# Kernel optimization log

Hardware: AMD Instinct MI355X
Metric: run time of the kernel (lower is better)

The kernel has to match this reference:

```python
import jax, jax.numpy as jnp
import numpy as np

B, N, C = 32, 2248, 1024
D = 128            # bottleneck (down_size)
P = 200            # num_prompt_tokens
SCALE = D ** (-0.5)


def setup_inputs() -> dict:
    key = jax.random.key(0)
    k = jax.random.split(key, 5)
    return {
        "x": jax.random.normal(k[0], (B, N, C), dtype=jnp.float32),
        "W_down": jax.random.normal(k[1], (C, D), dtype=jnp.float32) * (C ** -0.5),
        "b_down": jax.random.normal(k[2], (D,), dtype=jnp.float32) * 0.01,
        "W_up": jax.random.normal(k[3], (D, C), dtype=jnp.float32) * (D ** -0.5),
        "b_up": jax.random.normal(k[4], (C,), dtype=jnp.float32) * 0.01,
        "gate": jnp.ones((), dtype=jnp.float32),
    }


def reference(x, W_down, b_down, W_up, b_up, gate):
    # down-projection + exact GELU (torch nn.GELU default is erf-based)
    down = jax.nn.gelu(jnp.einsum('bnc,cd->bnd', x, W_down) + b_down,
                       approximate=False)                      # [B, N, D]
    prompt_down = down[:, :P, :]                               # [B, P, D]
    token_down = down[:, P:, :]                                # [B, N-P, D]
    # prompt-token cross attention
    attn = jax.nn.softmax(
        jnp.einsum('bpd,btd->bpt', prompt_down, token_down) * SCALE, axis=-1)
    prompt_out = jnp.einsum('bpt,btd->bpd', attn, token_down)  # [B, P, D]
    combined = jnp.concatenate([prompt_out, token_down], axis=1)  # [B, N, D]
    up = jnp.einsum('bnd,dc->bnc', combined, W_up) + b_up      # [B, N, C]
    return gate * up
```

## Files before the change

kernel.cpp:

```cpp
#include <hip/hip_runtime.h>
#include <hip/hip_bf16.h>
#include <math.h>

#define B_   32
#define N_   2248
#define C_   1024
#define D_   128
#define P_   200
#define T_   2048
#define M_   (B_ * N_)
#define SCALE_ 0.08838834764831845f

typedef __bf16 bf16;
typedef __bf16 bf16x8 __attribute__((ext_vector_type(8)));
typedef __bf16 bf16x4 __attribute__((ext_vector_type(4)));
typedef float  f32x4  __attribute__((ext_vector_type(4)));
typedef unsigned int u32x4 __attribute__((ext_vector_type(4)));

#define VT_COL(dd, t) ((((((t) >> 3) ^ (((dd) >> 3) & 7)) << 3)) | ((t) & 7))

__global__ void k_prep(const float* __restrict__ Wd, const float* __restrict__ Wu,
                       bf16* __restrict__ WtD, bf16* __restrict__ WtU) {
    int i = blockIdx.x * 256 + threadIdx.x;
    if (i >= 131072) return;
    int d = i >> 10, k = i & 1023;
    WtD[i] = (bf16)Wd[k * 128 + d];
    int c = i >> 7, e = i & 127;
    WtU[i] = (bf16)Wu[e * 1024 + c];
}

__launch_bounds__(256, 3)
__global__ void k_down(const float* __restrict__ x, const bf16* __restrict__ WtD,
                       const float* __restrict__ bd, bf16* __restrict__ down) {
    __shared__ bf16 As[128][72];
    const int tid = threadIdx.x;
    const int lane = tid & 63, wid = tid >> 6;
    const int wm = wid >> 1, wn = wid & 1;
    const int li = lane & 15, lg = lane >> 4;
    const int m0 = blockIdx.x * 128;
    const bf16* Bp = WtD + (size_t)(wn * 64 + li) * C_ + lg * 8;

    f32x4 acc[4][4];
    const f32x4 zero = {0.f, 0.f, 0.f, 0.f};
#pragma unroll
    for (int i = 0; i < 4; i++)
#pragma unroll
        for (int j = 0; j < 4; j++) acc[i][j] = zero;

    for (int k0 = 0; k0 < C_; k0 += 64) {
        __syncthreads();
#pragma unroll
        for (int it = 0; it < 4; it++) {
            int ch = tid + it * 256;
            int r = ch >> 3, c8 = (ch & 7) * 8;
            const float* src = x + (size_t)(m0 + r) * C_ + k0 + c8;
            f32x4 v0 = *(const f32x4*)src;
            f32x4 v1 = *(const f32x4*)(src + 4);
            bf16x8 o;
            o[0] = (bf16)v0[0]; o[1] = (bf16)v0[1]; o[2] = (bf16)v0[2]; o[3] = (bf16)v0[3];
            o[4] = (bf16)v1[0]; o[5] = (bf16)v1[1]; o[6] = (bf16)v1[2]; o[7] = (bf16)v1[3];
            *(bf16x8*)&As[r][c8] = o;
        }
        __syncthreads();
#pragma unroll
        for (int kk = 0; kk < 2; kk++) {
            bf16x8 af[4], bf_[4];
#pragma unroll
            for (int f = 0; f < 4; f++)
                bf_[f] = *(const bf16x8*)(Bp + (size_t)(f * 16) * C_ + k0 + kk * 32);
#pragma unroll
            for (int f = 0; f < 4; f++)
                af[f] = *(const bf16x8*)&As[wm * 64 + f * 16 + li][kk * 32 + lg * 8];
#pragma unroll
            for (int fm = 0; fm < 4; fm++)
#pragma unroll
                for (int fn = 0; fn < 4; fn++)
                    acc[fm][fn] = __builtin_amdgcn_mfma_f32_16x16x32_bf16(
                        af[fm], bf_[fn], acc[fm][fn], 0, 0, 0);
        }
    }
#pragma unroll
    for (int fn = 0; fn < 4; fn++) {
        int col = wn * 64 + fn * 16 + li;
        float bias = bd[col];
#pragma unroll
        for (int fm = 0; fm < 4; fm++) {
            int rb = m0 + wm * 64 + fm * 16 + lg * 4;
#pragma unroll
            for (int r = 0; r < 4; r++) {
                float v = acc[fm][fn][r] + bias;
                float g = 0.5f * v * (1.0f + erff(v * 0.70710678118654752f));
                down[(size_t)(rb + r) * D_ + col] = (bf16)g;
            }
        }
    }
}

__launch_bounds__(256, 2)
__global__ void k_attn(const bf16* __restrict__ down, float* __restrict__ Opart,
                       float* __restrict__ Mpart, float* __restrict__ Lpart) {
    __shared__ bf16 Qs[64][136];
    __shared__ bf16 Ks[64][136];
    __shared__ bf16 Vt[128][72];
    __shared__ bf16 Ps[4][16][72];
    const int tid = threadIdx.x;
    const int lane = tid & 63, w = tid >> 6;
    const int li = lane & 15, lg = lane >> 4;
    const int b  = blockIdx.x >> 3;
    const int qt = (blockIdx.x >> 1) & 3;
    const int th = blockIdx.x & 1;
    const size_t base = (size_t)b * N_ * D_;
    const int tbase = P_ + th * 1024;

#pragma unroll
    for (int it = 0; it < 4; it++) {
        int ch = tid + it * 256;
        int r = ch >> 4, c8 = (ch & 15) * 8;
        *(u32x4*)&Qs[r][c8] = *(const u32x4*)(down + base + (size_t)(qt * 64 + r) * D_ + c8);
    }
    __syncthreads();
    bf16x8 qf[4];
#pragma unroll
    for (int kk = 0; kk < 4; kk++)
        qf[kk] = *(const bf16x8*)&Qs[w * 16 + li][kk * 32 + lg * 8];

    float m_run[4], l_run[4];
    f32x4 acc[8];
    const f32x4 zero = {0.f, 0.f, 0.f, 0.f};
#pragma unroll
    for (int r = 0; r < 4; r++) { m_run[r] = -3.0e38f; l_run[r] = 0.f; }
#pragma unroll
    for (int fn = 0; fn < 8; fn++) acc[fn] = zero;

    for (int tt = 0; tt < 16; tt++) {
        __syncthreads();
#pragma unroll
        for (int it = 0; it < 4; it++) {
            int ch = tid + it * 256;
            int r = ch >> 4, c8 = (ch & 15) * 8;
            u32x4 v = *(const u32x4*)(down + base + (size_t)(tbase + tt * 64 + r) * D_ + c8);
            *(u32x4*)&Ks[r][c8] = v;
            bf16 tmp[8];
            *(u32x4*)tmp = v;
#pragma unroll
            for (int j = 0; j < 8; j++) Vt[c8 + j][VT_COL(c8 + j, r)] = tmp[j];
        }
        __syncthreads();
        f32x4 s[4];
#pragma unroll
        for (int fn = 0; fn < 4; fn++) {
            s[fn] = zero;
#pragma unroll
            for (int kk = 0; kk < 4; kk++) {
                bf16x8 kf = *(const bf16x8*)&Ks[fn * 16 + li][kk * 32 + lg * 8];
                s[fn] = __builtin_amdgcn_mfma_f32_16x16x32_bf16(qf[kk], kf, s[fn], 0, 0, 0);
            }
            s[fn] *= SCALE_;
        }
#pragma unroll
        for (int r = 0; r < 4; r++) {
            float tmax = fmaxf(fmaxf(s[0][r], s[1][r]), fmaxf(s[2][r], s[3][r]));
#pragma unroll
            for (int off = 1; off < 16; off <<= 1)
                tmax = fmaxf(tmax, __shfl_xor(tmax, off, 64));
            float mnew = fmaxf(m_run[r], tmax);
            float corr = __expf(m_run[r] - mnew);
            m_run[r] = mnew;
            float psum = 0.f;
#pragma unroll
            for (int fn = 0; fn < 4; fn++) {
                float p = __expf(s[fn][r] - mnew);
                psum += p;
                Ps[w][lg * 4 + r][fn * 16 + li] = (bf16)p;
            }
#pragma unroll
            for (int off = 1; off < 16; off <<= 1)
                psum += __shfl_xor(psum, off, 64);
            l_run[r] = l_run[r] * corr + psum;
#pragma unroll
            for (int fn = 0; fn < 8; fn++) acc[fn][r] *= corr;
        }
#pragma unroll
        for (int kk = 0; kk < 2; kk++) {
            bf16x8 pf = *(const bf16x8*)&Ps[w][li][kk * 32 + lg * 8];
#pragma unroll
            for (int fn = 0; fn < 8; fn++) {
                int d = fn * 16 + li;
                bf16x8 vf = *(const bf16x8*)&Vt[d][VT_COL(d, kk * 32 + lg * 8)];
                acc[fn] = __builtin_amdgcn_mfma_f32_16x16x32_bf16(pf, vf, acc[fn], 0, 0, 0);
            }
        }
    }
#pragma unroll
    for (int r = 0; r < 4; r++) {
        int q = qt * 64 + w * 16 + lg * 4 + r;
        size_t ro = ((size_t)(b * 2 + th) * 256 + q) * 128;
#pragma unroll
        for (int fn = 0; fn < 8; fn++)
            Opart[ro + fn * 16 + li] = acc[fn][r];
        if (li == 0) {
            Mpart[(b * 2 + th) * 256 + q] = m_run[r];
            Lpart[(b * 2 + th) * 256 + q] = l_run[r];
        }
    }
}

__global__ void k_comb(const float* __restrict__ Opart, const float* __restrict__ Mpart,
                       const float* __restrict__ Lpart, bf16* __restrict__ pout) {
    int gid = blockIdx.x * 256 + threadIdx.x;
    if (gid >= (B_ * P_ * D_) / 4) return;
    int e = gid * 4;
    int row = e >> 7;
    int col = e & 127;
    int b = row / P_;
    int q = row - b * P_;
    int i1 = (b * 2 + 0) * 256 + q;
    int i2 = (b * 2 + 1) * 256 + q;
    float m1 = Mpart[i1], m2 = Mpart[i2];
    float l1 = Lpart[i1], l2 = Lpart[i2];
    float m = fmaxf(m1, m2);
    float a1 = __expf(m1 - m), a2 = __expf(m2 - m);
    float inv = 1.0f / (l1 * a1 + l2 * a2);
    f32x4 o1 = *(const f32x4*)&Opart[(size_t)i1 * 128 + col];
    f32x4 o2 = *(const f32x4*)&Opart[(size_t)i2 * 128 + col];
    bf16x4 o;
#pragma unroll
    for (int j = 0; j < 4; j++)
        o[j] = (bf16)((o1[j] * a1 + o2[j] * a2) * inv);
    *(bf16x4*)&pout[(size_t)row * 128 + col] = o;
}

__launch_bounds__(256, 3)
__global__ void k_up(const bf16* __restrict__ down, const bf16* __restrict__ pout,
                     const bf16* __restrict__ WtU, const float* __restrict__ bu,
                     const float* __restrict__ gate, float* __restrict__ out) {
    __shared__ bf16 As[128][136];
    const int tid = threadIdx.x;
    const int lane = tid & 63, wid = tid >> 6;
    const int wm = wid >> 1, wn = wid & 1;
    const int li = lane & 15, lg = lane >> 4;
    int bid = blockIdx.x;
    int wg = (bid & 7) * 562 + (bid >> 3);
    const int mt = wg >> 3, nt = wg & 7;
    const int m0 = mt * 128, n0 = nt * 128;
    const bf16* Bp = WtU + (size_t)(n0 + wn * 64 + li) * D_ + lg * 8;

#pragma unroll
    for (int it = 0; it < 8; it++) {
        int ch = tid + it * 256;
        int r = ch >> 4, c8 = (ch & 15) * 8;
        int m = m0 + r;
        int bb = m / N_;
        int n = m - bb * N_;
        const bf16* src = (n < P_) ? (pout + (size_t)(bb * P_ + n) * D_ + c8)
                                   : (down + (size_t)m * D_ + c8);
        *(u32x4*)&As[r][c8] = *(const u32x4*)src;
    }
    __syncthreads();

    f32x4 acc[4][4];
    const f32x4 zero = {0.f, 0.f, 0.f, 0.f};
#pragma unroll
    for (int i = 0; i < 4; i++)
#pragma unroll
        for (int j = 0; j < 4; j++) acc[i][j] = zero;

#pragma unroll
    for (int kk = 0; kk < 4; kk++) {
        bf16x8 af[4], bf_[4];
#pragma unroll
        for (int f = 0; f < 4; f++)
            bf_[f] = *(const bf16x8*)(Bp + (size_t)(f * 16) * D_ + kk * 32);
#pragma unroll
        for (int f = 0; f < 4; f++)
            af[f] = *(const bf16x8*)&As[wm * 64 + f * 16 + li][kk * 32 + lg * 8];
#pragma unroll
        for (int fm = 0; fm < 4; fm++)
#pragma unroll
            for (int fn = 0; fn < 4; fn++)
                acc[fm][fn] = __builtin_amdgcn_mfma_f32_16x16x32_bf16(
                    af[fm], bf_[fn], acc[fm][fn], 0, 0, 0);
    }

    float g = gate[0];
#pragma unroll
    for (int fn = 0; fn < 4; fn++) {
        int c = n0 + wn * 64 + fn * 16 + li;
        float bias = bu[c];
#pragma unroll
        for (int fm = 0; fm < 4; fm++) {
            int rb = m0 + wm * 64 + fm * 16 + lg * 4;
#pragma unroll
            for (int r = 0; r < 4; r++)
                out[(size_t)(rb + r) * C_ + c] = g * (acc[fm][fn][r] + bias);
        }
    }
}

extern "C" void kernel_launch(void* const* d_in, const int* in_sizes, int n_in,
                              void* d_out, int out_size, void* d_ws, size_t ws_size,
                              hipStream_t stream) {
    const float* x    = (const float*)d_in[0];
    const float* Wd   = (const float*)d_in[1];
    const float* bd   = (const float*)d_in[2];
    const float* Wu   = (const float*)d_in[3];
    const float* bu   = (const float*)d_in[4];
    const float* gate = (const float*)d_in[5];
    float* out = (float*)d_out;

    char* w = (char*)d_ws;
    bf16*  down  = (bf16*)w;
    bf16*  pout  = (bf16*)(w + 18415616);
    bf16*  WtD   = (bf16*)(w + 20054016);
    bf16*  WtU   = (bf16*)(w + 20316160);
    float* Opart = (float*)(w + 20578304);
    float* Mpart = (float*)(w + 28966912);
    float* Lpart = (float*)(w + 29032448);

    k_prep<<<512, 256, 0, stream>>>(Wd, Wu, WtD, WtU);
    k_down<<<M_ / 128, 256, 0, stream>>>(x, WtD, bd, down);
    k_attn<<<B_ * 8, 256, 0, stream>>>(down, Opart, Mpart, Lpart);
    k_comb<<<800, 256, 0, stream>>>(Opart, Mpart, Lpart, pout);
    k_up<<<(M_ / 128) * 8, 256, 0, stream>>>(down, pout, WtU, bu, gate, out);
}
```

Baseline: 267.4 us.

## Load GEMM operands directly from global and split attention keys four ways

The down and up projection kernels stop staging the A tile in shared memory. Each lane now loads its MFMA fragment straight from global memory (converting fp32 to bf16 in k_down), which removes the LDS writes and barriers. The risk is redundant global loads across the two column-warps and less coalesced access. The attention kernel splits the key range into four chunks instead of two and uses an XCD-aware block remap, doubling the grid to 512 blocks. The combine kernel merges four partials, and the workspace offsets grow to fit them.

```diff
diff --git a/kernel.cpp b/kernel.cpp
--- a/kernel.cpp
+++ b/kernel.cpp
@@ -32,13 +32,13 @@
 __launch_bounds__(256, 3)
 __global__ void k_down(const float* __restrict__ x, const bf16* __restrict__ WtD,
                        const float* __restrict__ bd, bf16* __restrict__ down) {
-    __shared__ bf16 As[128][72];
     const int tid = threadIdx.x;
     const int lane = tid & 63, wid = tid >> 6;
     const int wm = wid >> 1, wn = wid & 1;
     const int li = lane & 15, lg = lane >> 4;
     const int m0 = blockIdx.x * 128;
-    const bf16* Bp = WtD + (size_t)(wn * 64 + li) * C_ + lg * 8;
+    const float* Ap = x   + (size_t)(m0 + wm * 64 + li) * C_ + lg * 8;
+    const bf16*  Bp = WtD + (size_t)(wn * 64 + li) * C_ + lg * 8;
 
     f32x4 acc[4][4];
     const f32x4 zero = {0.f, 0.f, 0.f, 0.f};
@@ -48,29 +48,20 @@
         for (int j = 0; j < 4; j++) acc[i][j] = zero;
 
     for (int k0 = 0; k0 < C_; k0 += 64) {
-        __syncthreads();
-#pragma unroll
-        for (int it = 0; it < 4; it++) {
-            int ch = tid + it * 256;
-            int r = ch >> 3, c8 = (ch & 7) * 8;
-            const float* src = x + (size_t)(m0 + r) * C_ + k0 + c8;
-            f32x4 v0 = *(const f32x4*)src;
-            f32x4 v1 = *(const f32x4*)(src + 4);
-            bf16x8 o;
-            o[0] = (bf16)v0[0]; o[1] = (bf16)v0[1]; o[2] = (bf16)v0[2]; o[3] = (bf16)v0[3];
-            o[4] = (bf16)v1[0]; o[5] = (bf16)v1[1]; o[6] = (bf16)v1[2]; o[7] = (bf16)v1[3];
-            *(bf16x8*)&As[r][c8] = o;
-        }
-        __syncthreads();
 #pragma unroll
         for (int kk = 0; kk < 2; kk++) {
             bf16x8 af[4], bf_[4];
 #pragma unroll
-            for (int f = 0; f < 4; f++)
+            for (int f = 0; f < 4; f++) {
+                const float* s = Ap + (size_t)(f * 16) * C_ + k0 + kk * 32;
+                f32x4 v0 = *(const f32x4*)s;
+                f32x4 v1 = *(const f32x4*)(s + 4);
+                bf16x8 o;
+                o[0] = (bf16)v0[0]; o[1] = (bf16)v0[1]; o[2] = (bf16)v0[2]; o[3] = (bf16)v0[3];
+                o[4] = (bf16)v1[0]; o[5] = (bf16)v1[1]; o[6] = (bf16)v1[2]; o[7] = (bf16)v1[3];
+                af[f] = o;
                 bf_[f] = *(const bf16x8*)(Bp + (size_t)(f * 16) * C_ + k0 + kk * 32);
-#pragma unroll
-            for (int f = 0; f < 4; f++)
-                af[f] = *(const bf16x8*)&As[wm * 64 + f * 16 + li][kk * 32 + lg * 8];
+            }
 #pragma unroll
             for (int fm = 0; fm < 4; fm++)
 #pragma unroll
@@ -106,11 +97,13 @@
     const int tid = threadIdx.x;
     const int lane = tid & 63, w = tid >> 6;
     const int li = lane & 15, lg = lane >> 4;
-    const int b  = blockIdx.x >> 3;
-    const int qt = (blockIdx.x >> 1) & 3;
-    const int th = blockIdx.x & 1;
+    const int bid = blockIdx.x;
+    const int wg = (bid & 7) * 64 + (bid >> 3);
+    const int b  = wg >> 4;
+    const int qt = (wg >> 2) & 3;
+    const int th = wg & 3;
     const size_t base = (size_t)b * N_ * D_;
-    const int tbase = P_ + th * 1024;
+    const int tbase = P_ + th * 512;
 
 #pragma unroll
     for (int it = 0; it < 4; it++) {
@@ -132,7 +125,7 @@
 #pragma unroll
     for (int fn = 0; fn < 8; fn++) acc[fn] = zero;
 
-    for (int tt = 0; tt < 16; tt++) {
+    for (int tt = 0; tt < 8; tt++) {
         __syncthreads();
 #pragma unroll
         for (int it = 0; it < 4; it++) {
@@ -194,13 +187,13 @@
 #pragma unroll
     for (int r = 0; r < 4; r++) {
         int q = qt * 64 + w * 16 + lg * 4 + r;
-        size_t ro = ((size_t)(b * 2 + th) * 256 + q) * 128;
+        size_t ro = ((size_t)(b * 4 + th) * 256 + q) * 128;
 #pragma unroll
         for (int fn = 0; fn < 8; fn++)
             Opart[ro + fn * 16 + li] = acc[fn][r];
         if (li == 0) {
-            Mpart[(b * 2 + th) * 256 + q] = m_run[r];
-            Lpart[(b * 2 + th) * 256 + q] = l_run[r];
+            Mpart[(b * 4 + th) * 256 + q] = m_run[r];
+            Lpart[(b * 4 + th) * 256 + q] = l_run[r];
         }
     }
 }
@@ -214,27 +207,35 @@
     int col = e & 127;
     int b = row / P_;
     int q = row - b * P_;
-    int i1 = (b * 2 + 0) * 256 + q;
-    int i2 = (b * 2 + 1) * 256 + q;
-    float m1 = Mpart[i1], m2 = Mpart[i2];
-    float l1 = Lpart[i1], l2 = Lpart[i2];
-    float m = fmaxf(m1, m2);
-    float a1 = __expf(m1 - m), a2 = __expf(m2 - m);
-    float inv = 1.0f / (l1 * a1 + l2 * a2);
-    f32x4 o1 = *(const f32x4*)&Opart[(size_t)i1 * 128 + col];
-    f32x4 o2 = *(const f32x4*)&Opart[(size_t)i2 * 128 + col];
-    bf16x4 o;
-#pragma unroll
-    for (int j = 0; j < 4; j++)
-        o[j] = (bf16)((o1[j] * a1 + o2[j] * a2) * inv);
-    *(bf16x4*)&pout[(size_t)row * 128 + col] = o;
+    float mm[4], ll[4];
+    float m = -3.0e38f;
+#pragma unroll
+    for (int t = 0; t < 4; t++) {
+        mm[t] = Mpart[(b * 4 + t) * 256 + q];
+        ll[t] = Lpart[(b * 4 + t) * 256 + q];
+        m = fmaxf(m, mm[t]);
+    }
+    float a[4], lsum = 0.f;
+#pragma unroll
+    for (int t = 0; t < 4; t++) { a[t] = __expf(mm[t] - m); lsum += ll[t] * a[t]; }
+    float inv = 1.0f / lsum;
+    f32x4 o = {0.f, 0.f, 0.f, 0.f};
+#pragma unroll
+    for (int t = 0; t < 4; t++) {
+        f32x4 ot = *(const f32x4*)&Opart[((size_t)(b * 4 + t) * 256 + q) * 128 + col];
+#pragma unroll
+        for (int j = 0; j < 4; j++) o[j] += ot[j] * a[t];
+    }
+    bf16x4 ob;
+#pragma unroll
+    for (int j = 0; j < 4; j++) ob[j] = (bf16)(o[j] * inv);
+    *(bf16x4*)&pout[(size_t)row * 128 + col] = ob;
 }
 
 __launch_bounds__(256, 3)
 __global__ void k_up(const bf16* __restrict__ down, const bf16* __restrict__ pout,
                      const bf16* __restrict__ WtU, const float* __restrict__ bu,
                      const float* __restrict__ gate, float* __restrict__ out) {
-    __shared__ bf16 As[128][136];
     const int tid = threadIdx.x;
     const int lane = tid & 63, wid = tid >> 6;
     const int wm = wid >> 1, wn = wid & 1;
@@ -243,20 +244,17 @@
     int wg = (bid & 7) * 562 + (bid >> 3);
     const int mt = wg >> 3, nt = wg & 7;
     const int m0 = mt * 128, n0 = nt * 128;
+
+    const bf16* rp[4];
+#pragma unroll
+    for (int f = 0; f < 4; f++) {
+        int row = m0 + wm * 64 + f * 16 + li;
+        int bb = row / N_;
+        int n = row - bb * N_;
+        rp[f] = (n < P_) ? (pout + (size_t)(bb * P_ + n) * D_ + lg * 8)
+                         : (down + (size_t)row * D_ + lg * 8);
+    }
     const bf16* Bp = WtU + (size_t)(n0 + wn * 64 + li) * D_ + lg * 8;
-
-#pragma unroll
-    for (int it = 0; it < 8; it++) {
-        int ch = tid + it * 256;
-        int r = ch >> 4, c8 = (ch & 15) * 8;
-        int m = m0 + r;
-        int bb = m / N_;
-        int n = m - bb * N_;
-        const bf16* src = (n < P_) ? (pout + (size_t)(bb * P_ + n) * D_ + c8)
-                                   : (down + (size_t)m * D_ + c8);
-        *(u32x4*)&As[r][c8] = *(const u32x4*)src;
-    }
-    __syncthreads();
 
     f32x4 acc[4][4];
     const f32x4 zero = {0.f, 0.f, 0.f, 0.f};
@@ -269,11 +267,10 @@
     for (int kk = 0; kk < 4; kk++) {
         bf16x8 af[4], bf_[4];
 #pragma unroll
-        for (int f = 0; f < 4; f++)
+        for (int f = 0; f < 4; f++) {
+            af[f]  = *(const bf16x8*)(rp[f] + kk * 32);
             bf_[f] = *(const bf16x8*)(Bp + (size_t)(f * 16) * D_ + kk * 32);
-#pragma unroll
-        for (int f = 0; f < 4; f++)
-            af[f] = *(const bf16x8*)&As[wm * 64 + f * 16 + li][kk * 32 + lg * 8];
+        }
 #pragma unroll
         for (int fm = 0; fm < 4; fm++)
 #pragma unroll
@@ -314,12 +311,12 @@
     bf16*  WtD   = (bf16*)(w + 20054016);
     bf16*  WtU   = (bf16*)(w + 20316160);
     float* Opart = (float*)(w + 20578304);
-    float* Mpart = (float*)(w + 28966912);
-    float* Lpart = (float*)(w + 29032448);
+    float* Mpart = (float*)(w + 37355520);
+    float* Lpart = (float*)(w + 37486592);
 
     k_prep<<<512, 256, 0, stream>>>(Wd, Wu, WtD, WtU);
     k_down<<<M_ / 128, 256, 0, stream>>>(x, WtD, bd, down);
-    k_attn<<<B_ * 8, 256, 0, stream>>>(down, Opart, Mpart, Lpart);
+    k_attn<<<512, 256, 0, stream>>>(down, Opart, Mpart, Lpart);
     k_comb<<<800, 256, 0, stream>>>(Opart, Mpart, Lpart, pout);
     k_up<<<(M_ / 128) * 8, 256, 0, stream>>>(down, pout, WtU, bu, gate, out);
 }
```

Measured after the change: 316.9 us. 18.5% more time.
